# Performance work log

Measured on AMD Instinct MI355X. Metric: run time of the kernel, lower is better.

Reference implementation:

```python
import jax, jax.numpy as jnp
import numpy as np

H = 4  # heads
NEG_SLOPE = 0.2


def gat_layer(feats, src, dst, W, a_src, a_dst, b, n_nodes):
    # feats: [N, Fin], W: [Fin, H*C], a_src/a_dst: [H, C], b: [C]
    C = a_src.shape[1]
    xh = (feats @ W).reshape(n_nodes, H, C)          # [N,H,C]
    alpha_s = (xh * a_src[None]).sum(-1)             # [N,H]
    alpha_d = (xh * a_dst[None]).sum(-1)             # [N,H]
    logits = alpha_s[src] + alpha_d[dst]             # [E,H]
    logits = jnp.where(logits >= 0, logits, NEG_SLOPE * logits)
    m = jax.ops.segment_max(logits, dst, num_segments=n_nodes)   # [N,H]
    m = jnp.where(jnp.isfinite(m), m, 0.0)
    e = jnp.exp(logits - m[dst])                     # [E,H]
    denom = jax.ops.segment_sum(e, dst, num_segments=n_nodes)    # [N,H]
    alpha = e / denom[dst]                           # [E,H]
    out = jax.ops.segment_sum(alpha[:, :, None] * xh[src], dst,
                              num_segments=n_nodes)  # [N,H,C]
    return out.mean(axis=1) + b                      # concat=False -> head mean


def setup_inputs() -> dict:
    key = jax.random.key(0)
    ks = jax.random.split(key, 16)
    N, E, P = 20000, 320000, 100000
    POS, FIN, HID = 2, 128, 128
    x = jax.random.normal(ks[0], (N, POS + FIN), dtype=jnp.float32)
    edge_index = jax.random.randint(ks[1], (2, E), 0, N, dtype=jnp.int64)
    idx = jax.random.randint(ks[2], (2, P), 0, N, dtype=jnp.int64)
    sc = 1.0 / np.sqrt(FIN)
    W1 = jax.random.normal(ks[3], (FIN, H * HID), dtype=jnp.float32) * sc
    a_src1 = jax.random.normal(ks[4], (H, HID), dtype=jnp.float32) * sc
    a_dst1 = jax.random.normal(ks[5], (H, HID), dtype=jnp.float32) * sc
    b1 = jnp.zeros((HID,), jnp.float32)
    W2 = jax.random.normal(ks[6], (HID, H * HID), dtype=jnp.float32) * sc
    a_src2 = jax.random.normal(ks[7], (H, HID), dtype=jnp.float32) * sc
    a_dst2 = jax.random.normal(ks[8], (H, HID), dtype=jnp.float32) * sc
    b2 = jnp.zeros((HID,), jnp.float32)
    fc_w = jax.random.normal(ks[9], (2, 1), dtype=jnp.float32) * 0.5
    fc_b = jnp.zeros((1,), jnp.float32)
    return {"x": x, "edge_index": edge_index, "idx": idx,
            "W1": W1, "a_src1": a_src1, "a_dst1": a_dst1, "b1": b1,
            "W2": W2, "a_src2": a_src2, "a_dst2": a_dst2, "b2": b2,
            "fc_w": fc_w, "fc_b": fc_b}


def reference(x, edge_index, idx, W1, a_src1, a_dst1, b1,
              W2, a_src2, a_dst2, b2, fc_w, fc_b):
    POS = 2
    N = x.shape[0]
    coors, feats = x[:, :POS], x[:, POS:]
    # PyG default: add self loops
    loops = jnp.arange(N, dtype=edge_index.dtype)
    src = jnp.concatenate([edge_index[0], loops])
    dst = jnp.concatenate([edge_index[1], loops])
    feats = gat_layer(feats, src, dst, W1, a_src1, a_dst1, b1, N)
    feats = gat_layer(feats, src, dst, W2, a_src2, a_dst2, b2, N)
    n1, n2 = feats[idx[0]], feats[idx[1]]            # [P,HID]
    p1, p2 = coors[idx[0]], coors[idx[1]]            # [P,POS]
    pos_enc = ((p1 - p2) ** 2).sum(-1, keepdims=True)  # [P,1]
    pred = (n1 * n2).sum(-1, keepdims=True)            # [P,1]
    out = jnp.concatenate([pred, pos_enc], axis=1) @ fc_w + fc_b  # [P,1]
    return out
```

## Files before the change

### kernel.cpp

```cpp
#include <hip/hip_runtime.h>
#include <hip/hip_fp16.h>

#define H 4
#define C 128
#define FOUT 512

typedef __attribute__((ext_vector_type(8))) short s16x8;
typedef __attribute__((ext_vector_type(4))) float f32x4;
typedef __attribute__((ext_vector_type(4))) int i32x4;
typedef __attribute__((ext_vector_type(2))) int i32x2;

__device__ int amd_buf_load_i32(i32x4 rsrc, int voffset, int soffset, int aux) __asm("llvm.amdgcn.raw.buffer.load.i32");
__device__ i32x2 amd_buf_load_i32x2(i32x4 rsrc, int voffset, int soffset, int aux) __asm("llvm.amdgcn.raw.buffer.load.v2i32");
__device__ i32x4 amd_buf_load_i32x4(i32x4 rsrc, int voffset, int soffset, int aux) __asm("llvm.amdgcn.raw.buffer.load.v4i32");

__device__ __forceinline__ i32x4 make_rsrc(const void* p, unsigned int bytes) {
    i32x4 r;
    r.x = (int)(unsigned int)(unsigned long long)p;
    r.y = (int)(unsigned int)(((unsigned long long)p) >> 32);
    r.z = (int)bytes;
    r.w = 0x00020000;
    return r;
}

__device__ __forceinline__ unsigned int f2bf_bits(float f) {
    unsigned int u = __float_as_uint(f);
    u += 0x7fffu + ((u >> 16) & 1u);
    return u >> 16;
}
__device__ __forceinline__ unsigned int pack2bf(unsigned int u0, unsigned int u1) {
    unsigned int r0 = (u0 + 0x7fffu + ((u0 >> 16) & 1u)) >> 16;
    unsigned int r1 = (u1 + 0x7fffu + ((u1 >> 16) & 1u)) & 0xffff0000u;
    return r0 | r1;
}
__device__ __forceinline__ unsigned int pack2bf_f(float a, float b) {
    return f2bf_bits(a) | (f2bf_bits(b) << 16);
}
__device__ __forceinline__ float bflo(unsigned int u) { return __uint_as_float(u << 16); }
__device__ __forceinline__ float bfhi(unsigned int u) { return __uint_as_float(u & 0xffff0000u); }
__device__ __forceinline__ float leaky(float x) { return (x >= 0.f) ? x : 0.2f * x; }
__device__ __forceinline__ __half2 u2h2(unsigned int u) {
    union { unsigned int u; __half2 h; } c; c.u = u; return c.h;
}
__device__ __forceinline__ unsigned int h22u(__half2 h) {
    union { __half2 h; unsigned int u; } c; c.h = h; return c.u;
}
__device__ __forceinline__ unsigned int pkrtz_bits(float a, float b) {
    auto v = __builtin_amdgcn_cvt_pkrtz(a, b);
    union { decltype(v) h; unsigned int u; } c; c.h = v; return c.u;
}

__global__ void prep_hist(const float* __restrict__ W1, const float* __restrict__ W2,
                          unsigned short* __restrict__ Wt1, unsigned short* __restrict__ Wt2,
                          int* __restrict__ counts, const int* __restrict__ ei, int E, int N) {
    int b = blockIdx.x;
    if (b < 256) {
        int i = b * 256 + threadIdx.x;
        if (i < 128 * 512) {
            int c = i >> 7, k = i & 127;
            Wt1[i] = (unsigned short)f2bf_bits(W1[(size_t)k * FOUT + c]);
            Wt2[i] = (unsigned short)f2bf_bits(W2[(size_t)k * FOUT + c]);
        }
    } else {
        int e = (b - 256) * 256 + threadIdx.x;
        int M = E + N;
        if (e < M) {
            int d = (e < E) ? ei[E + e] : (e - E);
            atomicAdd(&counts[d], 1);
        }
    }
}

__device__ __forceinline__ void scan_body(const int* __restrict__ counts,
                                          int* __restrict__ row_off,
                                          int* __restrict__ cursor, int N, int* part) {
    int t = threadIdx.x;
    int chunk = (((N + 255) >> 8) + 3) & ~3;
    int b = t * chunk; if (b > N) b = N;
    int e = b + chunk; if (e > N) e = N;
    int s = 0;
    int i = b;
    for (; i + 3 < e; i += 4) {
        int4 v = *(const int4*)&counts[i];
        s += v.x + v.y + v.z + v.w;
    }
    for (; i < e; ++i) s += counts[i];
    part[t] = s;
    __syncthreads();
    for (int off = 1; off < 256; off <<= 1) {
        int v = (t >= off) ? part[t - off] : 0;
        __syncthreads();
        part[t] += v;
        __syncthreads();
    }
    int run = (t == 0) ? 0 : part[t - 1];
    i = b;
    for (; i + 3 < e; i += 4) {
        int4 c = *(const int4*)&counts[i];
        int4 r;
        r.x = run; r.y = run + c.x; r.z = r.y + c.y; r.w = r.z + c.z;
        *(int4*)&row_off[i] = r;
        *(int4*)&cursor[i] = r;
        run = r.w + c.w;
    }
    for (; i < e; ++i) { row_off[i] = run; cursor[i] = run; run += counts[i]; }
    if (t == 255) row_off[N] = part[255];
}

__global__ void scatter_kernel(const int* __restrict__ ei, int E, int N,
                               int* __restrict__ cursor, int* __restrict__ csr_src) {
    int e = blockIdx.x * blockDim.x + threadIdx.x;
    int M = E + N;
    if (e >= M) return;
    int s = (e < E) ? ei[e] : (e - E);
    int d = (e < E) ? ei[E + e] : (e - E);
    int pos = atomicAdd(&cursor[d], 1);
    csr_src[pos] = s;
}

template <bool IS_X>
__device__ __forceinline__ void gemm_body(int h, int r0, const void* __restrict__ Asrc,
                                          const float* __restrict__ bias, int Nrows,
                                          const unsigned short* __restrict__ Bt,
                                          const float* __restrict__ a_src,
                                          const float* __restrict__ a_dst,
                                          unsigned short* __restrict__ Xh,
                                          float* __restrict__ alpha_s,
                                          float* __restrict__ alpha_d,
                                          int Npad, i32x4* __restrict__ AsTile,
                                          float (*albuf)[2][16][2][2]) {
    int t = threadIdx.x;
    int lane = t & 63;
    int wv = t >> 6;
    int wr = wv >> 1, wc = wv & 1;
    int lr = lane & 15;
    int ksel = lane >> 4;

    #pragma unroll
    for (int i = 0; i < 4; ++i) {
        int q = t + i * 256;
        int row = q >> 4, cb = q & 15;
        int gr = r0 + row;
        i32x4 v;
        if constexpr (IS_X) {
            i32x4 rA = make_rsrc(Asrc, (unsigned int)Nrows * 520u);
            int base = gr * 520 + 8 + cb * 32;
            i32x2 u0 = amd_buf_load_i32x2(rA, base, 0, 0);
            i32x2 u1 = amd_buf_load_i32x2(rA, base + 8, 0, 0);
            i32x2 u2 = amd_buf_load_i32x2(rA, base + 16, 0, 0);
            i32x2 u3 = amd_buf_load_i32x2(rA, base + 24, 0, 0);
            v.x = (int)pack2bf((unsigned int)u0.x, (unsigned int)u0.y);
            v.y = (int)pack2bf((unsigned int)u1.x, (unsigned int)u1.y);
            v.z = (int)pack2bf((unsigned int)u2.x, (unsigned int)u2.y);
            v.w = (int)pack2bf((unsigned int)u3.x, (unsigned int)u3.y);
        } else {
            if (gr < Nrows) {
                int chalf = cb >> 3;
                int c8 = (cb & 7) * 8;
                const uint4* hb = (const uint4*)Asrc;
                uint4 a0 = hb[((size_t)(0 + chalf) * Npad + gr) * 8 + (cb & 7)];
                uint4 a1 = hb[((size_t)(2 + chalf) * Npad + gr) * 8 + (cb & 7)];
                uint4 a2 = hb[((size_t)(4 + chalf) * Npad + gr) * 8 + (cb & 7)];
                uint4 a3 = hb[((size_t)(6 + chalf) * Npad + gr) * 8 + (cb & 7)];
                __half2 s0 = __hadd2(__hadd2(u2h2(a0.x), u2h2(a1.x)), __hadd2(u2h2(a2.x), u2h2(a3.x)));
                __half2 s1 = __hadd2(__hadd2(u2h2(a0.y), u2h2(a1.y)), __hadd2(u2h2(a2.y), u2h2(a3.y)));
                __half2 s2 = __hadd2(__hadd2(u2h2(a0.z), u2h2(a1.z)), __hadd2(u2h2(a2.z), u2h2(a3.z)));
                __half2 s3 = __hadd2(__hadd2(u2h2(a0.w), u2h2(a1.w)), __hadd2(u2h2(a2.w), u2h2(a3.w)));
                const float* bp = bias + chalf * 64 + c8;
                float4 b0 = *(const float4*)bp;
                float4 b1 = *(const float4*)(bp + 4);
                float2 f0 = __half22float2(s0), f1 = __half22float2(s1);
                float2 f2 = __half22float2(s2), f3 = __half22float2(s3);
                v.x = (int)pack2bf_f(0.25f * f0.x + b0.x, 0.25f * f0.y + b0.y);
                v.y = (int)pack2bf_f(0.25f * f1.x + b0.z, 0.25f * f1.y + b0.w);
                v.z = (int)pack2bf_f(0.25f * f2.x + b1.x, 0.25f * f2.y + b1.y);
                v.w = (int)pack2bf_f(0.25f * f3.x + b1.z, 0.25f * f3.y + b1.w);
            } else {
                v = (i32x4){0, 0, 0, 0};
            }
        }
        AsTile[row * 16 + (cb ^ (row & 7))] = v;
    }
    __syncthreads();

    f32x4 acc[2][4];
    #pragma unroll
    for (int i = 0; i < 2; ++i)
        #pragma unroll
        for (int j = 0; j < 4; ++j) acc[i][j] = (f32x4){0.f, 0.f, 0.f, 0.f};

    const s16x8* Bb = (const s16x8*)(Bt + (size_t)(h * 128 + wc * 64 + lr) * C);

    #pragma unroll
    for (int ks = 0; ks < 4; ++ks) {
        int cb = ks * 4 + ksel;
        s16x8 af[2], bf[4];
        #pragma unroll
        for (int i = 0; i < 2; ++i) {
            int rowl = wr * 32 + i * 16 + lr;
            af[i] = __builtin_bit_cast(s16x8, AsTile[rowl * 16 + (cb ^ (rowl & 7))]);
        }
        #pragma unroll
        for (int j = 0; j < 4; ++j) bf[j] = Bb[(size_t)(j * 16) * 16 + cb];
        #pragma unroll
        for (int i = 0; i < 2; ++i)
            #pragma unroll
            for (int j = 0; j < 4; ++j)
                acc[i][j] = __builtin_amdgcn_mfma_f32_16x16x32_bf16(bf[j], af[i], acc[i][j], 0, 0, 0);
    }

    float4 avj[4], dvj[4];
    #pragma unroll
    for (int j = 0; j < 4; ++j) {
        int cc = h * C + wc * 64 + j * 16 + ksel * 4;
        avj[j] = *(const float4*)&a_src[cc];
        dvj[j] = *(const float4*)&a_dst[cc];
    }

    unsigned short* slabp = Xh + (size_t)(h * 2 + wc) * Npad * 64;
    float ps[2] = {0.f, 0.f}, pd[2] = {0.f, 0.f};
    #pragma unroll
    for (int i = 0; i < 2; ++i) {
        int gr = r0 + wr * 32 + i * 16 + lr;
        #pragma unroll
        for (int j = 0; j < 4; ++j) {
            f32x4 a4 = acc[i][j];
            ps[i] += a4[0] * avj[j].x + a4[1] * avj[j].y + a4[2] * avj[j].z + a4[3] * avj[j].w;
            pd[i] += a4[0] * dvj[j].x + a4[1] * dvj[j].y + a4[2] * dvj[j].z + a4[3] * dvj[j].w;
            uint2 o;
            o.x = pkrtz_bits(a4[0], a4[1]);
            o.y = pkrtz_bits(a4[2], a4[3]);
            *(uint2*)(slabp + (size_t)gr * 64 + j * 16 + ksel * 4) = o;
        }
        ps[i] += __shfl_xor(ps[i], 16); ps[i] += __shfl_xor(ps[i], 32);
        pd[i] += __shfl_xor(pd[i], 16); pd[i] += __shfl_xor(pd[i], 32);
    }
    if (lane < 16) {
        #pragma unroll
        for (int i = 0; i < 2; ++i) {
            albuf[wr][i][lane][wc][0] = ps[i];
            albuf[wr][i][lane][wc][1] = pd[i];
        }
    }
    __syncthreads();

    if (t < 128) {
        int rid = t >> 1, which = t & 1;
        int wr2 = rid >> 5, rem = rid & 31, i2 = rem >> 4, l2 = rem & 15;
        float v = albuf[wr2][i2][l2][0][which] + albuf[wr2][i2][l2][1][which];
        int gr = r0 + wr2 * 32 + i2 * 16 + l2;
        if (gr < Nrows) {
            if (which) alpha_d[gr * H + h] = v;
            else       alpha_s[gr * H + h] = v;
        }
    }
}

__global__ __launch_bounds__(256) void gemm1_scan(const float* __restrict__ x, int N,
                                                  const unsigned short* __restrict__ Wt1,
                                                  const float* __restrict__ as1,
                                                  const float* __restrict__ ad1,
                                                  unsigned short* __restrict__ Xh,
                                                  float* __restrict__ alpha_s,
                                                  float* __restrict__ alpha_d, int Npad,
                                                  const int* __restrict__ counts,
                                                  int* __restrict__ row_off,
                                                  int* __restrict__ cursor) {
    __shared__ i32x4 AsTile[1024];
    __shared__ float albuf[2][2][16][2][2];
    int b = blockIdx.x;
    if (b == 0) {
        scan_body(counts, row_off, cursor, N, (int*)AsTile);
        return;
    }
    int gb = b - 1;
    gemm_body<true>(gb & 3, (gb >> 2) * 64, x, nullptr, N, Wt1, as1, ad1, Xh, alpha_s, alpha_d,
                    Npad, AsTile, albuf);
}

__global__ __launch_bounds__(256) void gemm2_kernel(const unsigned short* __restrict__ hout, int N,
                                                    const float* __restrict__ b1,
                                                    const unsigned short* __restrict__ Wt2,
                                                    const float* __restrict__ as2,
                                                    const float* __restrict__ ad2,
                                                    unsigned short* __restrict__ Xh,
                                                    float* __restrict__ alpha_s,
                                                    float* __restrict__ alpha_d, int Npad) {
    __shared__ i32x4 AsTile[1024];
    __shared__ float albuf[2][2][16][2][2];
    int gb = blockIdx.x;
    gemm_body<false>(gb & 3, (gb >> 2) * 64, hout, b1, N, Wt2, as2, ad2, Xh, alpha_s, alpha_d,
                     Npad, AsTile, albuf);
}

__global__ __launch_bounds__(256) void attn_kernel(const float4* __restrict__ as4,
                                                   const float4* __restrict__ ad4,
                                                   const int* __restrict__ row_off,
                                                   const int* __restrict__ csr_src,
                                                   unsigned int* __restrict__ pk, int N, int M) {
    int n = blockIdx.x * 4 + (threadIdx.x >> 6);
    if (n >= N) return;
    int l = threadIdx.x & 63;
    int beg = row_off[n], end = row_off[n + 1];
    float4 mx = make_float4(-1e30f, -1e30f, -1e30f, -1e30f);
    for (int e = beg + l; e < end; e += 64) {
        float4 a = as4[csr_src[e]];
        mx.x = fmaxf(mx.x, a.x); mx.y = fmaxf(mx.y, a.y);
        mx.z = fmaxf(mx.z, a.z); mx.w = fmaxf(mx.w, a.w);
    }
    #pragma unroll
    for (int off = 32; off >= 1; off >>= 1) {
        mx.x = fmaxf(mx.x, __shfl_xor(mx.x, off));
        mx.y = fmaxf(mx.y, __shfl_xor(mx.y, off));
        mx.z = fmaxf(mx.z, __shfl_xor(mx.z, off));
        mx.w = fmaxf(mx.w, __shfl_xor(mx.w, off));
    }
    float4 d = ad4[n];
    float4 m;
    m.x = leaky(mx.x + d.x); m.y = leaky(mx.y + d.y);
    m.z = leaky(mx.z + d.z); m.w = leaky(mx.w + d.w);
    for (int e = beg + l; e < end; e += 64) {
        int s = csr_src[e];
        float4 a = as4[s];
        unsigned int su = (unsigned int)s;
        unsigned int w0 = (unsigned int)__half_as_ushort(__float2half(__expf(leaky(a.x + d.x) - m.x)));
        unsigned int w1 = (unsigned int)__half_as_ushort(__float2half(__expf(leaky(a.y + d.y) - m.y)));
        unsigned int w2 = (unsigned int)__half_as_ushort(__float2half(__expf(leaky(a.z + d.z) - m.z)));
        unsigned int w3 = (unsigned int)__half_as_ushort(__float2half(__expf(leaky(a.w + d.w) - m.w)));
        pk[e]                 = (w0 << 16) | su;
        pk[(size_t)M + e]     = (w1 << 16) | su;
        pk[(size_t)2 * M + e] = (w2 << 16) | su;
        pk[(size_t)3 * M + e] = (w3 << 16) | su;
    }
}

__global__ __launch_bounds__(256) void aggregate_v11(const unsigned short* __restrict__ xh,
                                                     const unsigned int* __restrict__ pk,
                                                     const int* __restrict__ row_off,
                                                     unsigned short* __restrict__ hout,
                                                     int N, int Npad, int M) {
    int i = blockIdx.x;
    int slab = i & 7;
    int h = slab >> 1;
    int t = threadIdx.x;
    int wv = t >> 6;
    int lane = t & 63;
    int slot = lane >> 4;
    int l16 = lane & 15;
    int nbase = ((i >> 3) * 4 + wv) * 2;
    if (nbase >= N) return;

    i32x4 rx = make_rsrc(xh + (size_t)slab * Npad * 64, (unsigned int)Npad * 128u);
    i32x4 rp = make_rsrc(pk + (size_t)h * M, (unsigned int)M * 4u);
    int ld8 = l16 << 3;
    int slot4 = slot << 2;
    int nend = (nbase + 2 < N) ? nbase + 2 : N;

    for (int n = nbase; n < nend; ++n) {
        int beg = row_off[n], end = row_off[n + 1];
        __half2 acc01 = u2h2(0), acc23 = u2h2(0), den2 = u2h2(0);

        for (int ebase = beg; ebase < end; ebase += 64) {
            int p = amd_buf_load_i32(rp, (ebase + lane) << 2, 0, 0);
            int nrem = end - ebase;
            int jmax = ((nrem < 64 ? nrem : 64) + 7) >> 3;
            for (int j = 0; j < jmax; ++j) {
                int addr = (j << 5) + slot4;
                int sp0 = __builtin_amdgcn_ds_bpermute(addr, p);
                int sp1 = __builtin_amdgcn_ds_bpermute(addr + 16, p);
                int e0 = ebase + (j << 3) + slot;
                i32x2 ga = amd_buf_load_i32x2(rx, ((sp0 & 0xffff) << 7) + ld8, 0, 0);
                i32x2 gb = amd_buf_load_i32x2(rx, ((sp1 & 0xffff) << 7) + ld8, 0, 0);
                unsigned int wa2 = __builtin_amdgcn_perm(sp0, sp0, 0x03020302);
                unsigned int wb2 = __builtin_amdgcn_perm(sp1, sp1, 0x03020302);
                if (e0 >= end) wa2 = 0u;
                if (e0 + 4 >= end) wb2 = 0u;
                __half2 wha = u2h2(wa2), whb = u2h2(wb2);
                acc01 = __hfma2(wha, u2h2((unsigned int)ga.x), acc01);
                acc23 = __hfma2(wha, u2h2((unsigned int)ga.y), acc23);
                acc01 = __hfma2(whb, u2h2((unsigned int)gb.x), acc01);
                acc23 = __hfma2(whb, u2h2((unsigned int)gb.y), acc23);
                den2 = __hadd2(den2, wha);
                den2 = __hadd2(den2, whb);
            }
        }

        #pragma unroll
        for (int off = 16; off <= 32; off <<= 1) {
            acc01 = __hadd2(acc01, u2h2((unsigned int)__shfl_xor((int)h22u(acc01), off)));
            acc23 = __hadd2(acc23, u2h2((unsigned int)__shfl_xor((int)h22u(acc23), off)));
            den2  = __hadd2(den2,  u2h2((unsigned int)__shfl_xor((int)h22u(den2),  off)));
        }

        if (slot == 0) {
            float2 f01 = __half22float2(acc01);
            float2 f23 = __half22float2(acc23);
            float inv = 1.f / __half2float(__low2half(den2));
            uint2 o;
            o.x = pkrtz_bits(f01.x * inv, f01.y * inv);
            o.y = pkrtz_bits(f23.x * inv, f23.y * inv);
            ((uint2*)hout)[((size_t)slab * Npad + n) * 16 + l16] = o;
        }
    }
}

__global__ void combine_kernel(const unsigned short* __restrict__ hout,
                               const float* __restrict__ bias,
                               unsigned short* __restrict__ featsbf, int N, int Npad,
                               float* __restrict__ out, const float* __restrict__ fcb, int P) {
    int i = blockIdx.x * blockDim.x + threadIdx.x;
    if (i < P) out[i] = fcb[0];
    if (i >= N * 64) return;
    int n = i >> 6, c2 = i & 63;
    int chalf = c2 >> 5, ld = c2 & 31;
    const unsigned int* hp = (const unsigned int*)hout;
    float lo = 0.f, hi = 0.f;
    #pragma unroll
    for (int h = 0; h < 4; ++h) {
        unsigned int v = hp[((size_t)(h * 2 + chalf) * Npad + n) * 32 + ld];
        float2 f = __half22float2(u2h2(v));
        lo += f.x; hi += f.y;
    }
    lo = 0.25f * lo + bias[c2 * 2];
    hi = 0.25f * hi + bias[c2 * 2 + 1];
    ((unsigned int*)featsbf)[(size_t)n * 64 + c2] = f2bf_bits(lo) | (f2bf_bits(hi) << 16);
}

__global__ __launch_bounds__(256) void pair_kernel(const unsigned short* __restrict__ featsbf,
                                                   const float* __restrict__ x,
                                                   const int* __restrict__ idx, int P,
                                                   const float* __restrict__ fc_w,
                                                   float* __restrict__ out) {
    int chalf = blockIdx.x & 1;
    int p = (blockIdx.x >> 1) * 16 + (threadIdx.x >> 4);
    int l = threadIdx.x & 15;
    if (p >= P) return;
    int i0 = idx[p], i1 = idx[P + p];
    uint2 a = ((const uint2*)featsbf)[(size_t)i0 * 32 + chalf * 16 + l];
    uint2 b = ((const uint2*)featsbf)[(size_t)i1 * 32 + chalf * 16 + l];
    float s = bflo(a.x) * bflo(b.x) + bfhi(a.x) * bfhi(b.x)
            + bflo(a.y) * bflo(b.y) + bfhi(a.y) * bfhi(b.y);
    s += __shfl_xor(s, 1); s += __shfl_xor(s, 2);
    s += __shfl_xor(s, 4); s += __shfl_xor(s, 8);
    if (l == 0) {
        float v = fc_w[0] * s;
        if (chalf == 0) {
            float2 c0 = *(const float2*)&x[(size_t)i0 * 130];
            float2 c1 = *(const float2*)&x[(size_t)i1 * 130];
            float dx = c0.x - c1.x;
            float dy = c0.y - c1.y;
            v += fc_w[1] * (dx * dx + dy * dy);
        }
        atomicAdd(&out[p], v);
    }
}

extern "C" void kernel_launch(void* const* d_in, const int* in_sizes, int n_in,
                              void* d_out, int out_size, void* d_ws, size_t ws_size,
                              hipStream_t stream) {
    const float* x   = (const float*)d_in[0];
    const int*   ei  = (const int*)d_in[1];
    const int*   idx = (const int*)d_in[2];
    const float* W1  = (const float*)d_in[3];
    const float* as1 = (const float*)d_in[4];
    const float* ad1 = (const float*)d_in[5];
    const float* b1  = (const float*)d_in[6];
    const float* W2  = (const float*)d_in[7];
    const float* as2 = (const float*)d_in[8];
    const float* ad2 = (const float*)d_in[9];
    const float* b2  = (const float*)d_in[10];
    const float* fcw = (const float*)d_in[11];
    const float* fcb = (const float*)d_in[12];
    float* out = (float*)d_out;

    const int N = in_sizes[0] / 130;
    const int E = in_sizes[1] / 2;
    const int P = in_sizes[2] / 2;
    const int M = E + N;
    const int Npad = (N + 127) & ~127;

    char* ws = (char*)d_ws;
    size_t off = 0;
    auto alloc = [&](size_t bytes) -> void* {
        void* p = ws + off;
        off += (bytes + 255) & ~(size_t)255;
        return p;
    };
    unsigned short* xh_f16  = (unsigned short*)alloc((size_t)Npad * FOUT * 2);
    unsigned short* hout    = (unsigned short*)alloc((size_t)Npad * FOUT * 2);
    unsigned short* featsbf = (unsigned short*)alloc((size_t)Npad * C * 2);
    unsigned short* Wt1     = (unsigned short*)alloc((size_t)128 * FOUT * 2);
    unsigned short* Wt2     = (unsigned short*)alloc((size_t)128 * FOUT * 2);
    float*          alpha_s = (float*)alloc((size_t)N * H * 4);
    float*          alpha_d = (float*)alloc((size_t)N * H * 4);
    unsigned int*   pk      = (unsigned int*)alloc((size_t)M * H * 4);
    int*            row_off = (int*)alloc((size_t)(N + 1) * 4);
    int*            cursor  = (int*)alloc((size_t)N * 4);
    int*            counts  = (int*)alloc((size_t)N * 4);
    int*            csr_src = (int*)alloc((size_t)M * 4);

    const int histBlocks = (M + 255) / 256;
    const int gemmBlocks = 4 * (Npad / 64);
    int aggGrid = ((N + 7) / 8) * 8;
    int cmbGrid = (N * 64 + 255) / 256;

    hipMemsetAsync(counts, 0, (size_t)N * 4, stream);
    prep_hist<<<256 + histBlocks, 256, 0, stream>>>(W1, W2, Wt1, Wt2, counts, ei, E, N);
    gemm1_scan<<<1 + gemmBlocks, 256, 0, stream>>>(x, N, Wt1, as1, ad1, xh_f16,
                                                   alpha_s, alpha_d, Npad,
                                                   counts, row_off, cursor);
    scatter_kernel<<<histBlocks, 256, 0, stream>>>(ei, E, N, cursor, csr_src);

    attn_kernel<<<(N + 3) / 4, 256, 0, stream>>>((const float4*)alpha_s, (const float4*)alpha_d,
                                                 row_off, csr_src, pk, N, M);
    aggregate_v11<<<aggGrid, 256, 0, stream>>>(xh_f16, pk, row_off, hout, N, Npad, M);

    gemm2_kernel<<<gemmBlocks, 256, 0, stream>>>(hout, N, b1, Wt2, as2, ad2, xh_f16,
                                                 alpha_s, alpha_d, Npad);
    attn_kernel<<<(N + 3) / 4, 256, 0, stream>>>((const float4*)alpha_s, (const float4*)alpha_d,
                                                 row_off, csr_src, pk, N, M);
    aggregate_v11<<<aggGrid, 256, 0, stream>>>(xh_f16, pk, row_off, hout, N, Npad, M);
    combine_kernel<<<cmbGrid, 256, 0, stream>>>(hout, b2, featsbf, N, Npad, out, fcb, P);

    pair_kernel<<<((P + 15) / 16) * 2, 256, 0, stream>>>(featsbf, x, idx, P, fcw, out);
}
```

Baseline: 223.7 us.

## Fuse attention softmax weight computation into aggregation kernel, drop packed buffer

Removes the separate attn_kernel, which wrote packed fp16 weight plus source index per head into a global buffer. The aggregation kernel now loads csr_src and alpha_s itself, computes the per-destination max with a wave reduction, then computes the exp weights on the fly before the gather. This saves two kernel launches and the pk write/read traffic. In exchange, each of the 8 slab blocks per node redoes the softmax max and exp work, adding redundant loads and a second pass over the edges.

After: 225.4 us. Within noise of the previous version (+0.8%).

```diff
diff --git a/kernel.cpp b/kernel.cpp
--- a/kernel.cpp
+++ b/kernel.cpp
@@ -293,49 +293,10 @@
                      Npad, AsTile, albuf);
 }
 
-__global__ __launch_bounds__(256) void attn_kernel(const float4* __restrict__ as4,
-                                                   const float4* __restrict__ ad4,
-                                                   const int* __restrict__ row_off,
-                                                   const int* __restrict__ csr_src,
-                                                   unsigned int* __restrict__ pk, int N, int M) {
-    int n = blockIdx.x * 4 + (threadIdx.x >> 6);
-    if (n >= N) return;
-    int l = threadIdx.x & 63;
-    int beg = row_off[n], end = row_off[n + 1];
-    float4 mx = make_float4(-1e30f, -1e30f, -1e30f, -1e30f);
-    for (int e = beg + l; e < end; e += 64) {
-        float4 a = as4[csr_src[e]];
-        mx.x = fmaxf(mx.x, a.x); mx.y = fmaxf(mx.y, a.y);
-        mx.z = fmaxf(mx.z, a.z); mx.w = fmaxf(mx.w, a.w);
-    }
-    #pragma unroll
-    for (int off = 32; off >= 1; off >>= 1) {
-        mx.x = fmaxf(mx.x, __shfl_xor(mx.x, off));
-        mx.y = fmaxf(mx.y, __shfl_xor(mx.y, off));
-        mx.z = fmaxf(mx.z, __shfl_xor(mx.z, off));
-        mx.w = fmaxf(mx.w, __shfl_xor(mx.w, off));
-    }
-    float4 d = ad4[n];
-    float4 m;
-    m.x = leaky(mx.x + d.x); m.y = leaky(mx.y + d.y);
-    m.z = leaky(mx.z + d.z); m.w = leaky(mx.w + d.w);
-    for (int e = beg + l; e < end; e += 64) {
-        int s = csr_src[e];
-        float4 a = as4[s];
-        unsigned int su = (unsigned int)s;
-        unsigned int w0 = (unsigned int)__half_as_ushort(__float2half(__expf(leaky(a.x + d.x) - m.x)));
-        unsigned int w1 = (unsigned int)__half_as_ushort(__float2half(__expf(leaky(a.y + d.y) - m.y)));
-        unsigned int w2 = (unsigned int)__half_as_ushort(__float2half(__expf(leaky(a.z + d.z) - m.z)));
-        unsigned int w3 = (unsigned int)__half_as_ushort(__float2half(__expf(leaky(a.w + d.w) - m.w)));
-        pk[e]                 = (w0 << 16) | su;
-        pk[(size_t)M + e]     = (w1 << 16) | su;
-        pk[(size_t)2 * M + e] = (w2 << 16) | su;
-        pk[(size_t)3 * M + e] = (w3 << 16) | su;
-    }
-}
-
-__global__ __launch_bounds__(256) void aggregate_v11(const unsigned short* __restrict__ xh,
-                                                     const unsigned int* __restrict__ pk,
+__global__ __launch_bounds__(256) void aggregate_v12(const unsigned short* __restrict__ xh,
+                                                     const float* __restrict__ alpha_s,
+                                                     const float* __restrict__ alpha_d,
+                                                     const int* __restrict__ csr_src,
                                                      const int* __restrict__ row_off,
                                                      unsigned short* __restrict__ hout,
                                                      int N, int Npad, int M) {
@@ -351,17 +312,44 @@
     if (nbase >= N) return;
 
     i32x4 rx = make_rsrc(xh + (size_t)slab * Npad * 64, (unsigned int)Npad * 128u);
-    i32x4 rp = make_rsrc(pk + (size_t)h * M, (unsigned int)M * 4u);
+    i32x4 rc = make_rsrc(csr_src, (unsigned int)M * 4u);
+    i32x4 ra = make_rsrc(alpha_s, (unsigned int)N * 16u);
     int ld8 = l16 << 3;
     int slot4 = slot << 2;
+    int h4 = h << 2;
     int nend = (nbase + 2 < N) ? nbase + 2 : N;
 
     for (int n = nbase; n < nend; ++n) {
         int beg = row_off[n], end = row_off[n + 1];
+        float ad = alpha_d[n * H + h];
+
+        int s0 = amd_buf_load_i32(rc, (beg + lane) << 2, 0, 0);
+        float a0 = -1e30f;
+        if (beg + lane < end)
+            a0 = __uint_as_float((unsigned int)amd_buf_load_i32(ra, (s0 << 4) + h4, 0, 0));
+        float amax = a0;
+        for (int eb = beg + 64; eb < end; eb += 64) {
+            int s = amd_buf_load_i32(rc, (eb + lane) << 2, 0, 0);
+            if (eb + lane < end)
+                amax = fmaxf(amax, __uint_as_float((unsigned int)amd_buf_load_i32(ra, (s << 4) + h4, 0, 0)));
+        }
+        #pragma unroll
+        for (int off = 32; off >= 1; off >>= 1) amax = fmaxf(amax, __shfl_xor(amax, off));
+        float m = leaky(amax + ad);
+
         __half2 acc01 = u2h2(0), acc23 = u2h2(0), den2 = u2h2(0);
-
         for (int ebase = beg; ebase < end; ebase += 64) {
-            int p = amd_buf_load_i32(rp, (ebase + lane) << 2, 0, 0);
+            int s; float a;
+            if (ebase == beg) { s = s0; a = a0; }
+            else {
+                s = amd_buf_load_i32(rc, (ebase + lane) << 2, 0, 0);
+                a = (ebase + lane < end)
+                    ? __uint_as_float((unsigned int)amd_buf_load_i32(ra, (s << 4) + h4, 0, 0))
+                    : -1e30f;
+            }
+            float w = __expf(leaky(a + ad) - m);
+            int p = (int)(((unsigned int)__half_as_ushort(__float2half(w)) << 16) | (unsigned int)s);
+
             int nrem = end - ebase;
             int jmax = ((nrem < 64 ? nrem : 64) + 7) >> 3;
             for (int j = 0; j < jmax; ++j) {
@@ -493,7 +481,6 @@
     unsigned short* Wt2     = (unsigned short*)alloc((size_t)128 * FOUT * 2);
     float*          alpha_s = (float*)alloc((size_t)N * H * 4);
     float*          alpha_d = (float*)alloc((size_t)N * H * 4);
-    unsigned int*   pk      = (unsigned int*)alloc((size_t)M * H * 4);
     int*            row_off = (int*)alloc((size_t)(N + 1) * 4);
     int*            cursor  = (int*)alloc((size_t)N * 4);
     int*            counts  = (int*)alloc((size_t)N * 4);
@@ -511,15 +498,13 @@
                                                    counts, row_off, cursor);
     scatter_kernel<<<histBlocks, 256, 0, stream>>>(ei, E, N, cursor, csr_src);
 
-    attn_kernel<<<(N + 3) / 4, 256, 0, stream>>>((const float4*)alpha_s, (const float4*)alpha_d,
-                                                 row_off, csr_src, pk, N, M);
-    aggregate_v11<<<aggGrid, 256, 0, stream>>>(xh_f16, pk, row_off, hout, N, Npad, M);
+    aggregate_v12<<<aggGrid, 256, 0, stream>>>(xh_f16, alpha_s, alpha_d, csr_src, row_off,
+                                               hout, N, Npad, M);
 
     gemm2_kernel<<<gemmBlocks, 256, 0, stream>>>(hout, N, b1, Wt2, as2, ad2, xh_f16,
                                                  alpha_s, alpha_d, Npad);
-    attn_kernel<<<(N + 3) / 4, 256, 0, stream>>>((const float4*)alpha_s, (const float4*)alpha_d,
-                                                 row_off, csr_src, pk, N, M);
-    aggregate_v11<<<aggGrid, 256, 0, stream>>>(xh_f16, pk, row_off, hout, N, Npad, M);
+    aggregate_v12<<<aggGrid, 256, 0, stream>>>(xh_f16, alpha_s, alpha_d, csr_src, row_off,
+                                               hout, N, Npad, M);
     combine_kernel<<<cmbGrid, 256, 0, stream>>>(hout, b2, featsbf, N, Npad, out, fcb, P);
 
     pair_kernel<<<((P + 15) / 16) * 2, 256, 0, stream>>>(featsbf, x, idx, P, fcw, out);
```
